# Optimization experiments

Hardware: AMD Instinct MI355X
Metric: run time of the kernel (lower is better)

Reference implementation:

```python
import jax, jax.numpy as jnp
import numpy as np

N = 1_048_576   # collocation points
D_IN = 3        # seq_net[0]
H = 32          # hidden width (seq_net[1..3])
B = 4           # seq_net[-1] = number of parallel branches / outputs


def setup_inputs() -> dict:
    key = jax.random.key(0)
    ks = jax.random.split(key, 9)

    def init_w(k, shape, fan_in):
        bound = 1.0 / np.sqrt(fan_in)
        return jax.random.uniform(k, shape, jnp.float32, -bound, bound)

    x = jax.random.normal(ks[0], (N, D_IN), dtype=jnp.float32)
    # Per-branch weights stacked on leading branch axis B (torch.nn.Linear init ranges).
    W0 = init_w(ks[1], (B, D_IN, H), D_IN)
    b0 = init_w(ks[2], (B, H), D_IN)
    W1 = init_w(ks[3], (B, H, H), H)
    b1 = init_w(ks[4], (B, H), H)
    W2 = init_w(ks[5], (B, H, H), H)
    b2 = init_w(ks[6], (B, H), H)
    W3 = init_w(ks[7], (B, H, 1), H)
    b3 = init_w(ks[8], (B, 1), H)
    return {"x": x, "W0": W0, "b0": b0, "W1": W1, "b1": b1,
            "W2": W2, "b2": b2, "W3": W3, "b3": b3}


def reference(x, W0, b0, W1, b1, W2, b2, W3, b3):
    # All B branches computed as one batched GEMM chain (same math as the
    # python loop over per-branch Linear+tanh stacks in PFNN.forward).
    h = jnp.tanh(jnp.einsum('nd,bdh->bnh', x, W0) + b0[:, None, :])   # [B,N,H]
    h = jnp.tanh(jnp.einsum('bnd,bdh->bnh', h, W1) + b1[:, None, :])  # [B,N,H]
    h = jnp.tanh(jnp.einsum('bnd,bdh->bnh', h, W2) + b2[:, None, :])  # [B,N,H]
    out = jnp.einsum('bnd,bdh->bnh', h, W3) + b3[:, None, :]          # [B,N,1]
    # torch.cat(preds, dim=1): branch outputs side by side -> [N, B]
    return jnp.transpose(out[:, :, 0])
```

## Files before the change

### kernel.cpp

```cpp
#include <hip/hip_runtime.h>


#define NPTS 1048576
#define BLOCK 256
#define HROW 80
#define SCALE 2.8853900817779268f

#define OFF_BSC  16384
#define OFF_W0F  17408
#define OFF_B0P  25600
#define OFF_W3P  26112

using f16   = _Float16;
using f16x8 = __attribute__((ext_vector_type(8))) _Float16;
using f32x4 = __attribute__((ext_vector_type(4))) float;
using hfx2  = decltype(__builtin_amdgcn_cvt_pkrtz(0.0f, 0.0f));

__device__ __forceinline__ void inv4c(float v0, float v1, float v2, float v3,
                                      float& o0, float& o1, float& o2, float& o3)
{
    float a0 = __builtin_amdgcn_exp2f(v0) + 1.0f;
    float a1 = __builtin_amdgcn_exp2f(v1) + 1.0f;
    float a2 = __builtin_amdgcn_exp2f(v2) + 1.0f;
    float a3 = __builtin_amdgcn_exp2f(v3) + 1.0f;
    float p01 = a0 * a1;
    float p23 = a2 * a3;
    float p   = p01 * p23;
    float r   = __builtin_amdgcn_rcpf(p);
    float r01 = r * p23;
    float r23 = r * p01;
    o0 = __builtin_fmaf(r01, a1, -0.5f);
    o1 = __builtin_fmaf(r01, a0, -0.5f);
    o2 = __builtin_fmaf(r23, a3, -0.5f);
    o3 = __builtin_fmaf(r23, a2, -0.5f);
}

__device__ __forceinline__ void epi_mt(const f32x4& c0, const f32x4& c1, int mt,
                                       unsigned char* __restrict__ H,
                                       int col, int quad)
{
    #pragma unroll
    for (int r = 0; r < 4; r += 2) {
        int p = mt * 16 + quad * 4 + r;
        float o0, o1, o2, o3;
        inv4c(c0[r], c1[r], c0[r + 1], c1[r + 1], o0, o1, o2, o3);
        union { hfx2 h; unsigned int u; } cv0, cv1;
        cv0.h = __builtin_amdgcn_cvt_pkrtz(o0, o1);
        cv1.h = __builtin_amdgcn_cvt_pkrtz(o2, o3);
        *reinterpret_cast<unsigned int*>(H + p * HROW + 4 * col)       = cv0.u;
        *reinterpret_cast<unsigned int*>(H + (p + 1) * HROW + 4 * col) = cv1.u;
    }
}

__device__ __forceinline__ void layer0_block(int b, const f16x8 (&xfrag)[4],
                                             const f16* __restrict__ W0f,
                                             const float* __restrict__ B0p,
                                             unsigned char* __restrict__ H,
                                             int col, int quad)
{
    const f16* wb = W0f + (b * 2) * 512;
    f16x8 bf0 = *reinterpret_cast<const f16x8*>(wb + col * 32 + quad * 8);
    f16x8 bf1 = *reinterpret_cast<const f16x8*>(wb + 512 + col * 32 + quad * 8);
    const float2 bp = *reinterpret_cast<const float2*>(B0p + ((b * 16 + col) << 1));
    f32x4 ci0 = {bp.x, bp.x, bp.x, bp.x};
    f32x4 ci1 = {bp.y, bp.y, bp.y, bp.y};

    #pragma unroll
    for (int mt = 0; mt < 4; ++mt) {
        f32x4 c0 = __builtin_amdgcn_mfma_f32_16x16x32_f16(xfrag[mt], bf0, ci0, 0, 0, 0);
        f32x4 c1 = __builtin_amdgcn_mfma_f32_16x16x32_f16(xfrag[mt], bf1, ci1, 0, 0, 0);
        epi_mt(c0, c1, mt, H, col, quad);
    }
}

__device__ __forceinline__ void hidden_block(int l, int b,
                                             const f16* __restrict__ Wf,
                                             const float* __restrict__ Bsc,
                                             unsigned char* __restrict__ H,
                                             int col, int quad)
{
    const f16* wb = Wf + ((l * 4 + b) * 2) * 512;
    f16x8 bf0 = *reinterpret_cast<const f16x8*>(wb + col * 32 + quad * 8);
    f16x8 bf1 = *reinterpret_cast<const f16x8*>(wb + 512 + col * 32 + quad * 8);
    const float2 bp = *reinterpret_cast<const float2*>(
        Bsc + (((l * 4 + b) * 16 + col) << 1));
    f32x4 ci0 = {bp.x, bp.x, bp.x, bp.x};
    f32x4 ci1 = {bp.y, bp.y, bp.y, bp.y};

    #pragma unroll
    for (int mt = 0; mt < 4; ++mt) {
        const f16x8 av = *reinterpret_cast<const f16x8*>(
            H + (mt * 16 + col) * HROW + quad * 16);
        f32x4 c0 = __builtin_amdgcn_mfma_f32_16x16x32_f16(av, bf0, ci0, 0, 0, 0);
        f32x4 c1 = __builtin_amdgcn_mfma_f32_16x16x32_f16(av, bf1, ci1, 0, 0, 0);
        epi_mt(c0, c1, mt, H, col, quad);
    }
}

__device__ __forceinline__ float dot8(unsigned int ux, unsigned int uy,
                                      unsigned int uz, unsigned int uw,
                                      uint4 w, float acc)
{
#if __has_builtin(__builtin_amdgcn_fdot2)
    union { unsigned int uu; hfx2 hh; } a0, a1, a2, a3, b0, b1, b2, b3;
    a0.uu = ux; a1.uu = uy; a2.uu = uz; a3.uu = uw;
    b0.uu = w.x; b1.uu = w.y; b2.uu = w.z; b3.uu = w.w;
    acc = __builtin_amdgcn_fdot2(a0.hh, b0.hh, acc, false);
    acc = __builtin_amdgcn_fdot2(a1.hh, b1.hh, acc, false);
    acc = __builtin_amdgcn_fdot2(a2.hh, b2.hh, acc, false);
    acc = __builtin_amdgcn_fdot2(a3.hh, b3.hh, acc, false);
#else
    union { unsigned int uu; f16 h[2]; } a[4], bw[4];
    a[0].uu = ux; a[1].uu = uy; a[2].uu = uz; a[3].uu = uw;
    bw[0].uu = w.x; bw[1].uu = w.y; bw[2].uu = w.z; bw[3].uu = w.w;
    #pragma unroll
    for (int q = 0; q < 4; ++q) {
        acc = __builtin_fmaf((float)a[q].h[0], (float)bw[q].h[0], acc);
        acc = __builtin_fmaf((float)a[q].h[1], (float)bw[q].h[1], acc);
    }
#endif
    return acc;
}

__global__ void prep_kernel(const float* __restrict__ W0, const float* __restrict__ b0,
                            const float* __restrict__ W1, const float* __restrict__ b1,
                            const float* __restrict__ W2, const float* __restrict__ b2,
                            const float* __restrict__ W3,
                            unsigned char* __restrict__ ws)
{
    int i = blockIdx.x * 256 + threadIdx.x;
    if (i < 8192) {
        int k = i & 31, n = (i >> 5) & 15, t = (i >> 9) & 1, b = (i >> 10) & 3, l = i >> 12;
        int f = 2 * n + t;
        const float* W = l ? W2 : W1;
        reinterpret_cast<f16*>(ws)[i] = (f16)(-2.0f * SCALE * W[(b * 32 + k) * 32 + f]);
    } else if (i < 8448) {
        int j = i - 8192;
        int n = j & 15, t = (j >> 4) & 1, b = (j >> 5) & 3, l = j >> 7;
        const float* bb = l ? b2 : b1;
        reinterpret_cast<float*>(ws + OFF_BSC)[(((l * 4 + b) * 16 + n) << 1) | t]
            = SCALE * bb[b * 32 + 2 * n + t];
    } else if (i < 12544) {
        int j = i - 8448;
        int k = j & 31, n = (j >> 5) & 15, t = (j >> 9) & 1, b = (j >> 10) & 3;
        int f = 2 * n + t;
        int q = k >> 3, jj = k & 7;
        int row = -1; bool lo = false;
        if (q == 0 && jj < 6)      row = (jj < 3) ? jj : jj - 3;
        else if (q == 1 && jj < 3) { row = jj; lo = true; }
        f16 outv = (f16)0.0f;
        if (row >= 0) {
            float w  = SCALE * W0[(b * 3 + row) * 32 + f];
            f16   wh = (f16)w;
            outv = lo ? (f16)(w - (float)wh) : wh;
        }
        reinterpret_cast<f16*>(ws + OFF_W0F)[((b * 2 + t) * 16 + n) * 32 + k] = outv;
    } else if (i < 12672) {
        int j = i - 12544;
        int n = j & 15, t = (j >> 4) & 1, b = j >> 5;
        reinterpret_cast<float*>(ws + OFF_B0P)[(((b) * 16 + n) << 1) | t]
            = SCALE * b0[b * 32 + 2 * n + t];
    } else if (i < 12736) {
        int j = i - 12672;
        union { hfx2 h; unsigned int u; } cv;
        cv.h = __builtin_amdgcn_cvt_pkrtz(-2.0f * W3[2 * j], -2.0f * W3[2 * j + 1]);
        reinterpret_cast<unsigned int*>(ws + OFF_W3P)[j] = cv.u;
    }
}

__global__ __launch_bounds__(BLOCK, 8) void pfnn_kernel(
    const float* __restrict__ x, const unsigned char* __restrict__ ws,
    const float* __restrict__ b3,
    float* __restrict__ out)
{
    __shared__ __align__(16) unsigned char Hl[4][64 * HROW];

    const f16*   Wf  = reinterpret_cast<const f16*>(ws);
    const float* Bsc = reinterpret_cast<const float*>(ws + OFF_BSC);
    const f16*   W0f = reinterpret_cast<const f16*>(ws + OFF_W0F);
    const float* B0p = reinterpret_cast<const float*>(ws + OFF_B0P);
    const unsigned int* W3p = reinterpret_cast<const unsigned int*>(ws + OFF_W3P);

    const int t    = threadIdx.x;
    const int lane = t & 63;
    const int wv   = t >> 6;
    const int col  = lane & 15;
    const int quad = lane >> 4;
    unsigned char* __restrict__ H = &Hl[wv][0];

    const int n0 = blockIdx.x * BLOCK + t;
    const float x0 = x[3 * n0 + 0];
    const float x1 = x[3 * n0 + 1];
    const float x2 = x[3 * n0 + 2];

    f16x8 xfrag[4];
    {
        union { hfx2 h; int u; } q0_, q1_, q2_;
        q0_.h = __builtin_amdgcn_cvt_pkrtz(x0, x1);
        float r0 = x0 - (float)q0_.h[0];
        float r1 = x1 - (float)q0_.h[1];
        q1_.h = __builtin_amdgcn_cvt_pkrtz(x2, r0);
        float r2 = x2 - (float)q1_.h[0];
        q2_.h = __builtin_amdgcn_cvt_pkrtz(r1, r2);
        int d0 = q0_.u, d1 = q1_.u, d2 = q2_.u;
        #pragma unroll
        for (int mt = 0; mt < 4; ++mt) {
            int addr = 4 * (mt * 16 + col);
            union { int i[4]; f16x8 f; } u;
            u.i[0] = __builtin_amdgcn_ds_bpermute(addr, d0);
            u.i[1] = __builtin_amdgcn_ds_bpermute(addr, d1);
            u.i[2] = __builtin_amdgcn_ds_bpermute(addr, d2);
            u.i[3] = 0;
            xfrag[mt] = u.f;
        }
    }

    float res[4];
    const unsigned char* __restrict__ row = H + lane * HROW;

    layer0_block(0, xfrag, W0f, B0p, H, col, quad);

    #pragma unroll 1
    for (int b = 0; b < 3; ++b) {
        hidden_block(0, b, Wf, Bsc, H, col, quad);
        hidden_block(1, b, Wf, Bsc, H, col, quad);

        uint4 u0 = *reinterpret_cast<const uint4*>(row);
        uint4 u1 = *reinterpret_cast<const uint4*>(row + 16);
        uint4 u2 = *reinterpret_cast<const uint4*>(row + 32);
        uint4 u3 = *reinterpret_cast<const uint4*>(row + 48);

        layer0_block(b + 1, xfrag, W0f, B0p, H, col, quad);

        const uint4* wv4 = reinterpret_cast<const uint4*>(W3p + b * 16);
        uint4 w0 = wv4[0], w1 = wv4[1], w2 = wv4[2], w3v = wv4[3];
        float a0 = dot8(u0.x, u0.y, u0.z, u0.w, w0, b3[b]);
        float a1 = dot8(u1.x, u1.y, u1.z, u1.w, w1, 0.0f);
        float a2 = dot8(u2.x, u2.y, u2.z, u2.w, w2, 0.0f);
        float a3 = dot8(u3.x, u3.y, u3.z, u3.w, w3v, 0.0f);
        res[b] = (a0 + a1) + (a2 + a3);
    }

    {
        hidden_block(0, 3, Wf, Bsc, H, col, quad);
        hidden_block(1, 3, Wf, Bsc, H, col, quad);
        uint4 u0 = *reinterpret_cast<const uint4*>(row);
        uint4 u1 = *reinterpret_cast<const uint4*>(row + 16);
        uint4 u2 = *reinterpret_cast<const uint4*>(row + 32);
        uint4 u3 = *reinterpret_cast<const uint4*>(row + 48);
        const uint4* wv4 = reinterpret_cast<const uint4*>(W3p + 3 * 16);
        uint4 w0 = wv4[0], w1 = wv4[1], w2 = wv4[2], w3v = wv4[3];
        float a0 = dot8(u0.x, u0.y, u0.z, u0.w, w0, b3[3]);
        float a1 = dot8(u1.x, u1.y, u1.z, u1.w, w1, 0.0f);
        float a2 = dot8(u2.x, u2.y, u2.z, u2.w, w2, 0.0f);
        float a3 = dot8(u3.x, u3.y, u3.z, u3.w, w3v, 0.0f);
        res[3] = (a0 + a1) + (a2 + a3);
    }

    float4 r4 = make_float4(res[0], res[1], res[2], res[3]);
    *reinterpret_cast<float4*>(out + 4 * n0) = r4;
}

extern "C" void kernel_launch(void* const* d_in, const int* in_sizes, int n_in,
                              void* d_out, int out_size, void* d_ws, size_t ws_size,
                              hipStream_t stream) {
    const float* x  = (const float*)d_in[0];
    const float* W0 = (const float*)d_in[1];
    const float* b0 = (const float*)d_in[2];
    const float* W1 = (const float*)d_in[3];
    const float* b1 = (const float*)d_in[4];
    const float* W2 = (const float*)d_in[5];
    const float* b2 = (const float*)d_in[6];
    const float* W3 = (const float*)d_in[7];
    const float* b3 = (const float*)d_in[8];
    float* out = (float*)d_out;
    unsigned char* ws = (unsigned char*)d_ws;

    prep_kernel<<<dim3(50), dim3(256), 0, stream>>>(W0, b0, W1, b1, W2, b2, W3, ws);
    pfnn_kernel<<<dim3(NPTS / BLOCK), dim3(BLOCK), 0, stream>>>(x, ws, b3, out);
}
```

Before: 164.0 us.

## Pack tanh epilogue into float2 vector ops and un-skew layer0 from branch loop

Rewrites the tanh epilogue helper to use two-wide float vectors so the compiler can emit packed FP32 add/mul/fma instructions, cutting VALU instruction count in the epilogue. It also drops the software-pipelined placement of the next branch's layer-0 block (which was interleaved with the output-row LDS reads). The branch loop becomes a uniform four-iteration loop. This shrinks code and removes the peeled tail, but loses the overlap between the next layer-0 compute and the current output dot products.

```diff
diff --git a/kernel.cpp b/kernel.cpp
--- a/kernel.cpp
+++ b/kernel.cpp
@@ -14,25 +14,32 @@
 using f16   = _Float16;
 using f16x8 = __attribute__((ext_vector_type(8))) _Float16;
 using f32x4 = __attribute__((ext_vector_type(4))) float;
+using f32x2 = __attribute__((ext_vector_type(2))) float;
 using hfx2  = decltype(__builtin_amdgcn_cvt_pkrtz(0.0f, 0.0f));
 
 __device__ __forceinline__ void inv4c(float v0, float v1, float v2, float v3,
                                       float& o0, float& o1, float& o2, float& o3)
 {
-    float a0 = __builtin_amdgcn_exp2f(v0) + 1.0f;
-    float a1 = __builtin_amdgcn_exp2f(v1) + 1.0f;
-    float a2 = __builtin_amdgcn_exp2f(v2) + 1.0f;
-    float a3 = __builtin_amdgcn_exp2f(v3) + 1.0f;
-    float p01 = a0 * a1;
-    float p23 = a2 * a3;
-    float p   = p01 * p23;
-    float r   = __builtin_amdgcn_rcpf(p);
-    float r01 = r * p23;
-    float r23 = r * p01;
-    o0 = __builtin_fmaf(r01, a1, -0.5f);
-    o1 = __builtin_fmaf(r01, a0, -0.5f);
-    o2 = __builtin_fmaf(r23, a3, -0.5f);
-    o3 = __builtin_fmaf(r23, a2, -0.5f);
+    f32x2 x = {__builtin_amdgcn_exp2f(v0), __builtin_amdgcn_exp2f(v2)};
+    f32x2 y = {__builtin_amdgcn_exp2f(v1), __builtin_amdgcn_exp2f(v3)};
+    const f32x2 one2  = {1.0f, 1.0f};
+    const f32x2 negh2 = {-0.5f, -0.5f};
+    x = x + one2;
+    y = y + one2;
+    f32x2 P = x * y;
+    float p = P[0] * P[1];
+    float r = __builtin_amdgcn_rcpf(p);
+    f32x2 rr = {r, r};
+    f32x2 Ps = __builtin_shufflevector(P, P, 1, 0);
+    f32x2 R  = rr * Ps;
+#if __has_builtin(__builtin_elementwise_fma)
+    f32x2 o02 = __builtin_elementwise_fma(R, y, negh2);
+    f32x2 o13 = __builtin_elementwise_fma(R, x, negh2);
+#else
+    f32x2 o02 = {__builtin_fmaf(R[0], y[0], -0.5f), __builtin_fmaf(R[1], y[1], -0.5f)};
+    f32x2 o13 = {__builtin_fmaf(R[0], x[0], -0.5f), __builtin_fmaf(R[1], x[1], -0.5f)};
+#endif
+    o0 = o02[0]; o1 = o13[0]; o2 = o02[1]; o3 = o13[1];
 }
 
 __device__ __forceinline__ void epi_mt(const f32x4& c0, const f32x4& c1, int mt,
@@ -218,10 +225,9 @@
     float res[4];
     const unsigned char* __restrict__ row = H + lane * HROW;
 
-    layer0_block(0, xfrag, W0f, B0p, H, col, quad);
-
     #pragma unroll 1
-    for (int b = 0; b < 3; ++b) {
+    for (int b = 0; b < 4; ++b) {
+        layer0_block(b, xfrag, W0f, B0p, H, col, quad);
         hidden_block(0, b, Wf, Bsc, H, col, quad);
         hidden_block(1, b, Wf, Bsc, H, col, quad);
 
@@ -229,9 +235,6 @@
         uint4 u1 = *reinterpret_cast<const uint4*>(row + 16);
         uint4 u2 = *reinterpret_cast<const uint4*>(row + 32);
         uint4 u3 = *reinterpret_cast<const uint4*>(row + 48);
-
-        layer0_block(b + 1, xfrag, W0f, B0p, H, col, quad);
-
         const uint4* wv4 = reinterpret_cast<const uint4*>(W3p + b * 16);
         uint4 w0 = wv4[0], w1 = wv4[1], w2 = wv4[2], w3v = wv4[3];
         float a0 = dot8(u0.x, u0.y, u0.z, u0.w, w0, b3[b]);
@@ -239,22 +242,6 @@
         float a2 = dot8(u2.x, u2.y, u2.z, u2.w, w2, 0.0f);
         float a3 = dot8(u3.x, u3.y, u3.z, u3.w, w3v, 0.0f);
         res[b] = (a0 + a1) + (a2 + a3);
-    }
-
-    {
-        hidden_block(0, 3, Wf, Bsc, H, col, quad);
-        hidden_block(1, 3, Wf, Bsc, H, col, quad);
-        uint4 u0 = *reinterpret_cast<const uint4*>(row);
-        uint4 u1 = *reinterpret_cast<const uint4*>(row + 16);
-        uint4 u2 = *reinterpret_cast<const uint4*>(row + 32);
-        uint4 u3 = *reinterpret_cast<const uint4*>(row + 48);
-        const uint4* wv4 = reinterpret_cast<const uint4*>(W3p + 3 * 16);
-        uint4 w0 = wv4[0], w1 = wv4[1], w2 = wv4[2], w3v = wv4[3];
-        float a0 = dot8(u0.x, u0.y, u0.z, u0.w, w0, b3[3]);
-        float a1 = dot8(u1.x, u1.y, u1.z, u1.w, w1, 0.0f);
-        float a2 = dot8(u2.x, u2.y, u2.z, u2.w, w2, 0.0f);
-        float a3 = dot8(u3.x, u3.y, u3.z, u3.w, w3v, 0.0f);
-        res[3] = (a0 + a1) + (a2 + a3);
     }
 
     float4 r4 = make_float4(res[0], res[1], res[2], res[3]);
```

After: 148.5 us, median of 2. 9.4% less time.
